# Kernel tuning notes

Hardware: AMD Instinct MI355X
Metric: run time of the kernel (lower is better)

The kernel has to match this reference:

```python
import jax, jax.numpy as jnp
import numpy as np

N, E, D = 100000, 640000, 128

def setup_inputs() -> dict:
    key = jax.random.key(0)
    ks = jax.random.split(key, 12)
    s = 1.0 / np.sqrt(D)
    sg = 1.0 / np.sqrt(2 * D)
    return {
        "nodes": jax.random.normal(ks[0], (N, D), jnp.float32),
        "globals_": jax.random.normal(ks[1], (1, D), jnp.float32),
        "senders": jax.random.randint(ks[2], (E,), 0, N, jnp.int32),
        "receivers": jax.random.randint(ks[3], (E,), 0, N, jnp.int32),
        "W1_w": jax.random.normal(ks[4], (D, D), jnp.float32) * s,
        "W1_b": jnp.zeros((D,), jnp.float32),
        "W2_w": jax.random.normal(ks[5], (D, D), jnp.float32) * s,
        "W2_b": jnp.zeros((D,), jnp.float32),
        "W3_w": jax.random.normal(ks[6], (D, D), jnp.float32) * s,
        "W3_b": jnp.zeros((D,), jnp.float32),
        "Wg_w": jax.random.normal(ks[7], (2 * D, D), jnp.float32) * sg,
        "Wg_b": jnp.zeros((D,), jnp.float32),
    }


def reference(nodes, globals_, senders, receivers,
              W1_w, W1_b, W2_w, W2_b, W3_w, W3_b, Wg_w, Wg_b):
    n = nodes.shape[0]
    # W1 skip-branch projection
    h = nodes @ W1_w + W1_b                              # [N, D]
    # GraphConvolution: W2 projection + symmetric-normalized sum aggregation
    conv = nodes @ W2_w + W2_b                           # [N, D]
    ones = jnp.ones(senders.shape, conv.dtype)
    send_deg = jax.ops.segment_sum(ones, senders, num_segments=n)
    recv_deg = jax.ops.segment_sum(ones, receivers, num_segments=n)
    conv = conv * jax.lax.rsqrt(jnp.maximum(send_deg, 1.0))[:, None]
    agg = jax.ops.segment_sum(conv[senders], receivers, num_segments=n)  # gather + scatter
    agg = agg * jax.lax.rsqrt(jnp.maximum(recv_deg, 1.0))[:, None]
    h = h + agg
    # global -> node broadcast (globals is not None)
    h = h + (globals_[0:1] @ W3_w + W3_b)
    h = jax.nn.relu(h)
    h = h + nodes                                        # residual
    # global update: aggregate nodes (sum over single graph) + gated residual
    an = jnp.sum(h, axis=0, keepdims=True)               # [1, D]
    g_new = globals_ + jax.nn.relu(jnp.concatenate([an, globals_], axis=-1) @ Wg_w + Wg_b)
    return h, g_new
```

## Files before the change

### kernel.cpp

```cpp
#include <hip/hip_runtime.h>

#define D 128
#define AGGB 3136
#define MAXDEG 16
#define OVFCAP 16384

typedef __attribute__((ext_vector_type(8))) short short8;
typedef __attribute__((ext_vector_type(4))) float floatx4;

__device__ inline void bf16split(float x, ushort& hi, ushort& lo) {
  unsigned u = __float_as_uint(x);
  unsigned rh = (u + 0x7FFFu + ((u >> 16) & 1u)) & 0xFFFF0000u;
  hi = (ushort)(rh >> 16);
  float fl = x - __uint_as_float(rh);
  unsigned ul = __float_as_uint(fl);
  lo = (ushort)((ul + 0x7FFFu + ((ul >> 16) & 1u)) >> 16);
}

__device__ inline void place_edge(int s, int r, int p, int* __restrict__ srtp,
                                  int* __restrict__ ovf, int* __restrict__ ovfn) {
  if (p < MAXDEG) {
    srtp[r * MAXDEG + p] = s;
  } else {
    const int q = atomicAdd(ovfn, 1);
    if (q < OVFCAP) {
      ovf[2 * q] = r;
      ovf[2 * q + 1] = s;
    }
  }
}

__global__ void k_prep(const float* __restrict__ g, const float* __restrict__ W3,
                       const float* __restrict__ b3, float* __restrict__ gvec,
                       const float* __restrict__ W1, const float* __restrict__ W2,
                       ushort* __restrict__ wt) {
  const int b = blockIdx.x;
  if (b == 0) {
    __shared__ float part[256];
    const int j = threadIdx.x & 127, half = threadIdx.x >> 7;
    float acc = 0.f;
    for (int k = half * 64; k < half * 64 + 64; ++k)
      acc = fmaf(g[k], W3[k * D + j], acc);
    part[threadIdx.x] = acc;
    __syncthreads();
    if (threadIdx.x < D) gvec[j] = b3[j] + part[j] + part[j + 128];
    return;
  }
  const int id = (b - 1) * 256 + threadIdx.x;
  const int mat = id >> 14, idx = id & 16383;
  const int k = idx >> 7, nn = idx & 127;
  const float x = (mat ? W2 : W1)[k * D + nn];
  ushort hi, lo;
  bf16split(x, hi, lo);
  wt[(size_t)mat * 32768 + (size_t)nn * 128 + k] = hi;
  wt[(size_t)mat * 32768 + 16384 + (size_t)nn * 128 + k] = lo;
}

__global__ __launch_bounds__(256, 6) void k_eg(
    const int* __restrict__ snd, const int* __restrict__ rcv,
    int* __restrict__ cs, int* __restrict__ cr, int* __restrict__ srtp,
    int* __restrict__ ovf, int* __restrict__ ovfn, int E, int nbE4,
    const float* __restrict__ A, const ushort* __restrict__ wt,
    float* __restrict__ h1, int n) {
  const int b = blockIdx.x, t = threadIdx.x;
  if (b < nbE4) {
    const int e0 = b * 1024 + t * 4;
    if (e0 + 3 < E) {
      const int4 s4 = *(const int4*)(snd + e0);
      const int4 r4 = *(const int4*)(rcv + e0);
      atomicAdd(cs + s4.x, 1);
      atomicAdd(cs + s4.y, 1);
      atomicAdd(cs + s4.z, 1);
      atomicAdd(cs + s4.w, 1);
      const int p0 = atomicAdd(cr + r4.x, 1);
      const int p1 = atomicAdd(cr + r4.y, 1);
      const int p2 = atomicAdd(cr + r4.z, 1);
      const int p3 = atomicAdd(cr + r4.w, 1);
      place_edge(s4.x, r4.x, p0, srtp, ovf, ovfn);
      place_edge(s4.y, r4.y, p1, srtp, ovf, ovfn);
      place_edge(s4.z, r4.z, p2, srtp, ovf, ovfn);
      place_edge(s4.w, r4.w, p3, srtp, ovf, ovfn);
    } else {
      for (int e = e0; e < E && e < e0 + 4; ++e) {
        const int s = snd[e], r = rcv[e];
        atomicAdd(cs + s, 1);
        place_edge(s, r, atomicAdd(cr + r, 1), srtp, ovf, ovfn);
      }
    }
    return;
  }
  __shared__ ushort As[2 * 2 * 2560];
  const int row0 = (b - nbE4) * 64;
  const int lane = t & 63, w = t >> 6;
  const int m = lane & 15, quad = lane >> 4;

  floatx4 acc[4][2];
#pragma unroll
  for (int i = 0; i < 4; ++i)
#pragma unroll
    for (int j = 0; j < 2; ++j) acc[i][j] = (floatx4)0.f;

  const int srow = t >> 2, ko = (t & 3) * 8;
  const int grow = min(row0 + srow, n - 1);
  const float* Ag = A + (size_t)grow * D + ko;
  const int sa = srow * 40 + ko;

  float4 f0, f1;
#define LOADP(p)                              \
  {                                           \
    f0 = *(const float4*)(Ag + (p) * 32);     \
    f1 = *(const float4*)(Ag + (p) * 32 + 4); \
  }
#define STOREB(buf)                                               \
  {                                                               \
    ushort h0, l0, h1_, l1_, h2, l2, h3, l3;                      \
    ushort* Bp = &As[(buf) * 5120];                               \
    bf16split(f0.x, h0, l0); bf16split(f0.y, h1_, l1_);           \
    bf16split(f0.z, h2, l2); bf16split(f0.w, h3, l3);             \
    *(ushort4*)&Bp[sa] = make_ushort4(h0, h1_, h2, h3);           \
    *(ushort4*)&Bp[2560 + sa] = make_ushort4(l0, l1_, l2, l3);    \
    bf16split(f1.x, h0, l0); bf16split(f1.y, h1_, l1_);           \
    bf16split(f1.z, h2, l2); bf16split(f1.w, h3, l3);             \
    *(ushort4*)&Bp[sa + 4] = make_ushort4(h0, h1_, h2, h3);       \
    *(ushort4*)&Bp[2560 + sa + 4] = make_ushort4(l0, l1_, l2, l3);\
  }

  LOADP(0);
  STOREB(0);
  LOADP(1);
  __syncthreads();

  for (int p = 0; p < 4; ++p) {
    if (p < 3) STOREB((p + 1) & 1);
    if (p < 2) LOADP(p + 2);
    const ushort* Ab = &As[(p & 1) * 5120];
#pragma unroll
    for (int j = 0; j < 2; ++j) {
      const ushort* g1 = wt + (size_t)(w * 32 + j * 16 + m) * 128 + p * 32 + quad * 8;
      const short8 w1h = *(const short8*)g1;
      const short8 w1l = *(const short8*)(g1 + 16384);
#pragma unroll
      for (int i = 0; i < 4; ++i) {
        const int r = (i * 16 + m) * 40 + quad * 8;
        const short8 a1h = *(const short8*)&Ab[r];
        const short8 a1l = *(const short8*)&Ab[2560 + r];
        floatx4 c = acc[i][j];
        c = __builtin_amdgcn_mfma_f32_16x16x32_bf16(a1h, w1h, c, 0, 0, 0);
        c = __builtin_amdgcn_mfma_f32_16x16x32_bf16(a1h, w1l, c, 0, 0, 0);
        c = __builtin_amdgcn_mfma_f32_16x16x32_bf16(a1l, w1h, c, 0, 0, 0);
        acc[i][j] = c;
      }
    }
    __syncthreads();
  }
#undef LOADP
#undef STOREB

#pragma unroll
  for (int i = 0; i < 4; ++i)
#pragma unroll
    for (int pp = 0; pp < 4; ++pp) {
      const int rg = row0 + i * 16 + quad * 4 + pp;
      if (rg >= n) continue;
#pragma unroll
      for (int j = 0; j < 2; ++j)
        h1[(size_t)rg * D + w * 32 + j * 16 + m] = acc[i][j][pp];
    }
}

__global__ __launch_bounds__(256) void k_agg(
    const float* __restrict__ nodes, int* __restrict__ cnt_recv,
    const int* __restrict__ cnt_send, const int* __restrict__ srtp,
    const int* __restrict__ ovf, const int* __restrict__ ovfn,
    ushort* __restrict__ yh, ushort* __restrict__ yl, int n) {
  float* cf = (float*)cnt_recv;
  const int hw = threadIdx.x >> 5, ln = threadIdx.x & 31;
  const int ghw = blockIdx.x * 8 + hw;
  const int nhw = AGGB * 8;
  const int c0 = ln * 4;

  for (int r0 = ghw; r0 < n; r0 += 2 * nhw) {
    const int r1 = r0 + nhw;
    const bool has1 = r1 < n;
    const int dg0 = cnt_recv[r0];
    const int dg1 = has1 ? cnt_recv[r1] : 0;
    const int base0 = r0 * MAXDEG;
    const int base1 = (has1 ? r1 : 0) * MAXDEG;

    const int4 qa0 = *(const int4*)(srtp + base0);
    const int4 qb0 = *(const int4*)(srtp + base0 + 4);
    const int4 qa1 = *(const int4*)(srtp + base1);
    const int4 qb1 = *(const int4*)(srtp + base1 + 4);
    int idx0[8] = {qa0.x, qa0.y, qa0.z, qa0.w, qb0.x, qb0.y, qb0.z, qb0.w};
    int idx1[8] = {qa1.x, qa1.y, qa1.z, qa1.w, qb1.x, qb1.y, qb1.z, qb1.w};
#pragma unroll
    for (int j = 0; j < 8; ++j) {
      idx0[j] = (j < dg0) ? idx0[j] : 0;
      idx1[j] = (j < dg1) ? idx1[j] : 0;
    }
    float4 g0[8], g1[8];
#pragma unroll
    for (int j = 0; j < 8; ++j)
      g0[j] = *(const float4*)(nodes + (size_t)idx0[j] * D + c0);
#pragma unroll
    for (int j = 0; j < 8; ++j)
      g1[j] = *(const float4*)(nodes + (size_t)idx1[j] * D + c0);
    float rs0[8], rs1[8];
#pragma unroll
    for (int j = 0; j < 8; ++j) {
      rs0[j] = (j < dg0) ? rsqrtf(fmaxf((float)cnt_send[idx0[j]], 1.f)) : 0.f;
      rs1[j] = (j < dg1) ? rsqrtf(fmaxf((float)cnt_send[idx1[j]], 1.f)) : 0.f;
    }

    float sx0 = 0.f, sy0 = 0.f, sz0 = 0.f, sw0 = 0.f, cs0 = 0.f;
    float sx1 = 0.f, sy1 = 0.f, sz1 = 0.f, sw1 = 0.f, cs1 = 0.f;
#pragma unroll
    for (int j = 0; j < 8; ++j) {
      sx0 = fmaf(rs0[j], g0[j].x, sx0);
      sy0 = fmaf(rs0[j], g0[j].y, sy0);
      sz0 = fmaf(rs0[j], g0[j].z, sz0);
      sw0 = fmaf(rs0[j], g0[j].w, sw0);
      cs0 += rs0[j];
      sx1 = fmaf(rs1[j], g1[j].x, sx1);
      sy1 = fmaf(rs1[j], g1[j].y, sy1);
      sz1 = fmaf(rs1[j], g1[j].z, sz1);
      sw1 = fmaf(rs1[j], g1[j].w, sw1);
      cs1 += rs1[j];
    }
    for (int i = 8; i < min(dg0, MAXDEG); ++i) {
      const int s = srtp[base0 + i];
      const float r = rsqrtf(fmaxf((float)cnt_send[s], 1.f));
      const float4 c = *(const float4*)(nodes + (size_t)s * D + c0);
      sx0 = fmaf(r, c.x, sx0); sy0 = fmaf(r, c.y, sy0);
      sz0 = fmaf(r, c.z, sz0); sw0 = fmaf(r, c.w, sw0);
      cs0 += r;
    }
    for (int i = 8; i < min(dg1, MAXDEG); ++i) {
      const int s = srtp[base1 + i];
      const float r = rsqrtf(fmaxf((float)cnt_send[s], 1.f));
      const float4 c = *(const float4*)(nodes + (size_t)s * D + c0);
      sx1 = fmaf(r, c.x, sx1); sy1 = fmaf(r, c.y, sy1);
      sz1 = fmaf(r, c.z, sz1); sw1 = fmaf(r, c.w, sw1);
      cs1 += r;
    }
    if (dg0 > MAXDEG) {
      const int novf = min(*ovfn, OVFCAP);
      for (int k2 = 0; k2 < novf; ++k2) {
        if (ovf[2 * k2] == r0) {
          const int s = ovf[2 * k2 + 1];
          const float r = rsqrtf(fmaxf((float)cnt_send[s], 1.f));
          const float4 c = *(const float4*)(nodes + (size_t)s * D + c0);
          sx0 = fmaf(r, c.x, sx0); sy0 = fmaf(r, c.y, sy0);
          sz0 = fmaf(r, c.z, sz0); sw0 = fmaf(r, c.w, sw0);
          cs0 += r;
        }
      }
    }
    if (dg1 > MAXDEG) {
      const int novf = min(*ovfn, OVFCAP);
      for (int k2 = 0; k2 < novf; ++k2) {
        if (ovf[2 * k2] == r1) {
          const int s = ovf[2 * k2 + 1];
          const float r = rsqrtf(fmaxf((float)cnt_send[s], 1.f));
          const float4 c = *(const float4*)(nodes + (size_t)s * D + c0);
          sx1 = fmaf(r, c.x, sx1); sy1 = fmaf(r, c.y, sy1);
          sz1 = fmaf(r, c.z, sz1); sw1 = fmaf(r, c.w, sw1);
          cs1 += r;
        }
      }
    }

    {
      const float rr = rsqrtf(fmaxf((float)dg0, 1.f));
      ushort h0, l0, h1, l1, h2, l2, h3, l3;
      bf16split(sx0 * rr, h0, l0);
      bf16split(sy0 * rr, h1, l1);
      bf16split(sz0 * rr, h2, l2);
      bf16split(sw0 * rr, h3, l3);
      *(ushort4*)(yh + (size_t)r0 * D + c0) = make_ushort4(h0, h1, h2, h3);
      *(ushort4*)(yl + (size_t)r0 * D + c0) = make_ushort4(l0, l1, l2, l3);
      if (ln == 0) cf[r0] = rr * cs0;
    }
    if (has1) {
      const float rr = rsqrtf(fmaxf((float)dg1, 1.f));
      ushort h0, l0, h1, l1, h2, l2, h3, l3;
      bf16split(sx1 * rr, h0, l0);
      bf16split(sy1 * rr, h1, l1);
      bf16split(sz1 * rr, h2, l2);
      bf16split(sw1 * rr, h3, l3);
      *(ushort4*)(yh + (size_t)r1 * D + c0) = make_ushort4(h0, h1, h2, h3);
      *(ushort4*)(yl + (size_t)r1 * D + c0) = make_ushort4(l0, l1, l2, l3);
      if (ln == 0) cf[r1] = rr * cs1;
    }
  }
}

__global__ __launch_bounds__(256, 6) void k_gemm2(
    const float* __restrict__ A, const ushort* __restrict__ yh,
    const ushort* __restrict__ yl, const ushort* __restrict__ wt,
    const float* __restrict__ b1, const float* __restrict__ b2,
    const float* __restrict__ gvec, const float* __restrict__ cf,
    float* hio, float* __restrict__ an, int n) {
  __shared__ ushort As[2 * 2 * 2560];
  const int t = threadIdx.x;
  const int row0 = blockIdx.x * 64;
  const int lane = t & 63, w = t >> 6;
  const int m = lane & 15, quad = lane >> 4;

  floatx4 acc[4][2];
#pragma unroll
  for (int i = 0; i < 4; ++i)
#pragma unroll
    for (int j = 0; j < 2; ++j) acc[i][j] = (floatx4)0.f;

  const int srow = t >> 2, ko = (t & 3) * 8;
  const int grow = min(row0 + srow, n - 1);
  const ushort* yhb = yh + (size_t)grow * D + ko;
  const ushort* ylb = yl + (size_t)grow * D + ko;
  const int sa = srow * 40 + ko;

  uint4 r2, r3;
#define LOADP(p)                          \
  {                                       \
    r2 = *(const uint4*)(yhb + (p) * 32); \
    r3 = *(const uint4*)(ylb + (p) * 32); \
  }
#define STOREB(buf)                 \
  {                                 \
    ushort* Bp = &As[(buf) * 5120]; \
    *(uint4*)&Bp[sa] = r2;          \
    *(uint4*)&Bp[2560 + sa] = r3;   \
  }

  LOADP(0);
  STOREB(0);
  LOADP(1);
  __syncthreads();

  for (int p = 0; p < 4; ++p) {
    if (p < 3) STOREB((p + 1) & 1);
    if (p < 2) LOADP(p + 2);
    const ushort* Ab = &As[(p & 1) * 5120];
#pragma unroll
    for (int j = 0; j < 2; ++j) {
      const ushort* g2 =
          wt + 32768 + (size_t)(w * 32 + j * 16 + m) * 128 + p * 32 + quad * 8;
      const short8 w2h = *(const short8*)g2;
      const short8 w2l = *(const short8*)(g2 + 16384);
#pragma unroll
      for (int i = 0; i < 4; ++i) {
        const int r = (i * 16 + m) * 40 + quad * 8;
        const short8 a2h = *(const short8*)&Ab[r];
        const short8 a2l = *(const short8*)&Ab[2560 + r];
        floatx4 c = acc[i][j];
        c = __builtin_amdgcn_mfma_f32_16x16x32_bf16(a2h, w2h, c, 0, 0, 0);
        c = __builtin_amdgcn_mfma_f32_16x16x32_bf16(a2h, w2l, c, 0, 0, 0);
        c = __builtin_amdgcn_mfma_f32_16x16x32_bf16(a2l, w2h, c, 0, 0, 0);
        acc[i][j] = c;
      }
    }
    __syncthreads();
  }
#undef LOADP
#undef STOREB

  float bb[2], b2c[2];
#pragma unroll
  for (int j = 0; j < 2; ++j) {
    const int col = w * 32 + j * 16 + m;
    bb[j] = b1[col] + gvec[col];
    b2c[j] = b2[col];
  }
  float asum[2] = {0.f, 0.f};
#pragma unroll
  for (int i = 0; i < 4; ++i)
#pragma unroll
    for (int pp = 0; pp < 4; ++pp) {
      const int rg = row0 + i * 16 + quad * 4 + pp;
      if (rg >= n) continue;
      const float crv = cf[rg];
#pragma unroll
      for (int j = 0; j < 2; ++j) {
        const int col = w * 32 + j * 16 + m;
        float v = acc[i][j][pp] + bb[j] + crv * b2c[j] + hio[(size_t)rg * D + col];
        v = fmaxf(v, 0.f) + A[(size_t)rg * D + col];
        hio[(size_t)rg * D + col] = v;
        asum[j] += v;
      }
    }
#pragma unroll
  for (int j = 0; j < 2; ++j) {
    float v = asum[j];
    v += __shfl_xor(v, 16);
    v += __shfl_xor(v, 32);
    if (lane < 16) atomicAdd(an + w * 32 + j * 16 + m, v);
  }
}

__global__ void k_gupdate(const float* __restrict__ an, const float* __restrict__ g,
                          const float* __restrict__ Wg, const float* __restrict__ bg,
                          float* __restrict__ gout) {
  __shared__ float part[256];
  const int j = threadIdx.x & 127, half = threadIdx.x >> 7;
  float acc = 0.f;
  if (half == 0) {
    for (int k = 0; k < D; ++k) acc = fmaf(an[k], Wg[k * D + j], acc);
  } else {
    for (int k = 0; k < D; ++k) acc = fmaf(g[k], Wg[(D + k) * D + j], acc);
  }
  part[threadIdx.x] = acc;
  __syncthreads();
  if (threadIdx.x < D)
    gout[j] = g[j] + fmaxf(bg[j] + part[j] + part[j + 128], 0.f);
}

extern "C" void kernel_launch(void* const* d_in, const int* in_sizes, int n_in,
                              void* d_out, int out_size, void* d_ws, size_t ws_size,
                              hipStream_t stream) {
  const float* nodes = (const float*)d_in[0];
  const float* globals_ = (const float*)d_in[1];
  const int* senders = (const int*)d_in[2];
  const int* receivers = (const int*)d_in[3];
  const float* W1_w = (const float*)d_in[4];
  const float* W1_b = (const float*)d_in[5];
  const float* W2_w = (const float*)d_in[6];
  const float* W2_b = (const float*)d_in[7];
  const float* W3_w = (const float*)d_in[8];
  const float* W3_b = (const float*)d_in[9];
  const float* Wg_w = (const float*)d_in[10];
  const float* Wg_b = (const float*)d_in[11];
  const int N = in_sizes[0] / D;
  const int E = in_sizes[2];
  const int nbE4 = (E + 1023) / 1024;
  const int NG = (N + 63) / 64;

  float* h = (float*)d_out;
  float* gout = h + (size_t)N * D;

  float* ws = (float*)d_ws;
  ushort* yh = (ushort*)ws;
  ushort* yl = yh + (size_t)N * D;
  int* cnt_send = (int*)(yl + (size_t)N * D);
  int* cnt_recv = cnt_send + N;
  float* an = (float*)(cnt_recv + N);
  int* ovfn = (int*)(an + D);
  float* gvec = (float*)(ovfn + 64);
  int* srtp = (int*)(gvec + D);
  int* ovf = srtp + (size_t)N * MAXDEG;
  ushort* wt = (ushort*)(ovf + 2 * OVFCAP);

  (void)hipMemsetAsync(cnt_send, 0, (size_t)(2 * N + D + 64) * sizeof(int), stream);

  hipLaunchKernelGGL(k_prep, dim3(129), dim3(256), 0, stream,
                     globals_, W3_w, W3_b, gvec, W1_w, W2_w, wt);
  hipLaunchKernelGGL(k_eg, dim3(nbE4 + NG), dim3(256), 0, stream,
                     senders, receivers, cnt_send, cnt_recv, srtp, ovf, ovfn,
                     E, nbE4, nodes, wt, h, N);
  hipLaunchKernelGGL(k_agg, dim3(AGGB), dim3(256), 0, stream,
                     nodes, cnt_recv, cnt_send, srtp, ovf, ovfn, yh, yl, N);
  hipLaunchKernelGGL(k_gemm2, dim3(NG), dim3(256), 0, stream,
                     nodes, yh, yl, wt, W1_b, W2_b, gvec,
                     (const float*)cnt_recv, h, an, N);
  hipLaunchKernelGGL(k_gupdate, dim3(1), dim3(256), 0, stream, an, globals_,
                     Wg_w, Wg_b, gout);
}
```

Measured before the change: 376.5 us.

## Fuse all stages into one persistent kernel with grid barriers and merged GEMM

Replaces the five-kernel pipeline with a single persistent kernel of 512 blocks that uses atomic grid-wide barriers between the prep, edge-bucketing, aggregation and GEMM phases. It also merges the two GEMMs (nodes@W1 and agg@W2) into one pass, so the intermediate h is no longer written and re-read. The goal is to remove launch gaps and one full N×D round trip. In exchange, the edge-bucketing work no longer overlaps with the first GEMM. The spin barriers assume all 512 blocks are co-resident (2 per CU), which risks deadlock if that does not hold, and the fixed grid may underuse the GPU in some phases.

```diff
diff --git a/kernel.cpp b/kernel.cpp
--- a/kernel.cpp
+++ b/kernel.cpp
@@ -1,9 +1,9 @@
 #include <hip/hip_runtime.h>
 
 #define D 128
-#define AGGB 3136
 #define MAXDEG 16
 #define OVFCAP 16384
+#define GRID 512
 
 typedef __attribute__((ext_vector_type(8))) short short8;
 typedef __attribute__((ext_vector_type(4))) float floatx4;
@@ -17,8 +17,8 @@
   lo = (ushort)((ul + 0x7FFFu + ((ul >> 16) & 1u)) >> 16);
 }
 
-__device__ inline void place_edge(int s, int r, int p, int* __restrict__ srtp,
-                                  int* __restrict__ ovf, int* __restrict__ ovfn) {
+__device__ inline void place_edge(int s, int r, int p, int* srtp, int* ovf,
+                                  int* ovfn) {
   if (p < MAXDEG) {
     srtp[r * MAXDEG + p] = s;
   } else {
@@ -30,41 +30,59 @@
   }
 }
 
-__global__ void k_prep(const float* __restrict__ g, const float* __restrict__ W3,
-                       const float* __restrict__ b3, float* __restrict__ gvec,
-                       const float* __restrict__ W1, const float* __restrict__ W2,
-                       ushort* __restrict__ wt) {
-  const int b = blockIdx.x;
-  if (b == 0) {
-    __shared__ float part[256];
-    const int j = threadIdx.x & 127, half = threadIdx.x >> 7;
+__device__ inline void gbar(int* bar, int target) {
+  __syncthreads();
+  if (threadIdx.x == 0) {
+    __hip_atomic_fetch_add(bar, 1, __ATOMIC_RELEASE, __HIP_MEMORY_SCOPE_AGENT);
+    while (__hip_atomic_load(bar, __ATOMIC_ACQUIRE, __HIP_MEMORY_SCOPE_AGENT) <
+           target)
+      __builtin_amdgcn_s_sleep(2);
+  }
+  __syncthreads();
+}
+
+__global__ __launch_bounds__(256, 2) void k_mega(
+    const float* __restrict__ nodes, const float* __restrict__ g,
+    const int* __restrict__ snd, const int* __restrict__ rcv,
+    const float* __restrict__ W1, const float* __restrict__ b1,
+    const float* __restrict__ W2, const float* __restrict__ b2,
+    const float* __restrict__ W3, const float* __restrict__ b3,
+    const float* __restrict__ Wg, const float* __restrict__ bg,
+    int* cs, int* cr, float* an, int* ctrl, float* gvec, int* srtp, int* ovf,
+    ushort* wt, ushort* yh, ushort* yl, float* h, float* gout, int E, int n) {
+  __shared__ ushort As[2 * 4 * 2560];
+  int* ovfn = ctrl;
+  int* bar = ctrl + 1;
+  const int b = blockIdx.x, t = threadIdx.x;
+  const int gtid = b * 256 + t;
+  const int lane = t & 63, w = t >> 6;
+  const int m = lane & 15, quad = lane >> 4;
+  const int nbE4 = (E + 1023) / 1024;
+  const int nT = (n + 63) / 64;
+
+  if (gtid < 32768) {
+    const int mat = gtid >> 14, idx = gtid & 16383;
+    const int k = idx >> 7, nn = idx & 127;
+    const float x = (mat ? W2 : W1)[k * D + nn];
+    ushort hi, lo;
+    bf16split(x, hi, lo);
+    wt[(size_t)mat * 32768 + (size_t)nn * 128 + k] = hi;
+    wt[(size_t)mat * 32768 + 16384 + (size_t)nn * 128 + k] = lo;
+  }
+  if (b == GRID - 1) {
+    float* part = (float*)As;
+    const int j = t & 127, half = t >> 7;
     float acc = 0.f;
     for (int k = half * 64; k < half * 64 + 64; ++k)
       acc = fmaf(g[k], W3[k * D + j], acc);
-    part[threadIdx.x] = acc;
+    part[t] = acc;
     __syncthreads();
-    if (threadIdx.x < D) gvec[j] = b3[j] + part[j] + part[j + 128];
-    return;
-  }
-  const int id = (b - 1) * 256 + threadIdx.x;
-  const int mat = id >> 14, idx = id & 16383;
-  const int k = idx >> 7, nn = idx & 127;
-  const float x = (mat ? W2 : W1)[k * D + nn];
-  ushort hi, lo;
-  bf16split(x, hi, lo);
-  wt[(size_t)mat * 32768 + (size_t)nn * 128 + k] = hi;
-  wt[(size_t)mat * 32768 + 16384 + (size_t)nn * 128 + k] = lo;
-}
-
-__global__ __launch_bounds__(256, 6) void k_eg(
-    const int* __restrict__ snd, const int* __restrict__ rcv,
-    int* __restrict__ cs, int* __restrict__ cr, int* __restrict__ srtp,
-    int* __restrict__ ovf, int* __restrict__ ovfn, int E, int nbE4,
-    const float* __restrict__ A, const ushort* __restrict__ wt,
-    float* __restrict__ h1, int n) {
-  const int b = blockIdx.x, t = threadIdx.x;
-  if (b < nbE4) {
-    const int e0 = b * 1024 + t * 4;
+    if (t < D) gvec[j] = b3[j] + part[j] + part[j + 128];
+  }
+  gbar(bar, GRID);
+
+  for (int c = b; c < nbE4; c += GRID) {
+    const int e0 = c * 1024 + t * 4;
     if (e0 + 3 < E) {
       const int4 s4 = *(const int4*)(snd + e0);
       const int4 r4 = *(const int4*)(rcv + e0);
@@ -87,34 +105,167 @@
         place_edge(s, r, atomicAdd(cr + r, 1), srtp, ovf, ovfn);
       }
     }
-    return;
-  }
-  __shared__ ushort As[2 * 2 * 2560];
-  const int row0 = (b - nbE4) * 64;
-  const int lane = t & 63, w = t >> 6;
-  const int m = lane & 15, quad = lane >> 4;
-
-  floatx4 acc[4][2];
-#pragma unroll
-  for (int i = 0; i < 4; ++i)
-#pragma unroll
-    for (int j = 0; j < 2; ++j) acc[i][j] = (floatx4)0.f;
-
-  const int srow = t >> 2, ko = (t & 3) * 8;
-  const int grow = min(row0 + srow, n - 1);
-  const float* Ag = A + (size_t)grow * D + ko;
-  const int sa = srow * 40 + ko;
-
-  float4 f0, f1;
+  }
+  gbar(bar, 2 * GRID);
+
+  {
+    float* cf = (float*)cr;
+    const int hw = t >> 5, ln = t & 31;
+    const int ghw = b * 8 + hw;
+    const int nhw = GRID * 8;
+    const int c0 = ln * 4;
+    for (int r0 = ghw; r0 < n; r0 += 2 * nhw) {
+      const int r1 = r0 + nhw;
+      const bool has1 = r1 < n;
+      const int dg0 = cr[r0];
+      const int dg1 = has1 ? cr[r1] : 0;
+      const int base0 = r0 * MAXDEG;
+      const int base1 = (has1 ? r1 : 0) * MAXDEG;
+
+      const int4 qa0 = *(const int4*)(srtp + base0);
+      const int4 qb0 = *(const int4*)(srtp + base0 + 4);
+      const int4 qa1 = *(const int4*)(srtp + base1);
+      const int4 qb1 = *(const int4*)(srtp + base1 + 4);
+      int idx0[8] = {qa0.x, qa0.y, qa0.z, qa0.w, qb0.x, qb0.y, qb0.z, qb0.w};
+      int idx1[8] = {qa1.x, qa1.y, qa1.z, qa1.w, qb1.x, qb1.y, qb1.z, qb1.w};
+#pragma unroll
+      for (int j = 0; j < 8; ++j) {
+        idx0[j] = (j < dg0) ? idx0[j] : 0;
+        idx1[j] = (j < dg1) ? idx1[j] : 0;
+      }
+      float4 g0[8], g1[8];
+#pragma unroll
+      for (int j = 0; j < 8; ++j)
+        g0[j] = *(const float4*)(nodes + (size_t)idx0[j] * D + c0);
+#pragma unroll
+      for (int j = 0; j < 8; ++j)
+        g1[j] = *(const float4*)(nodes + (size_t)idx1[j] * D + c0);
+      float rs0[8], rs1[8];
+#pragma unroll
+      for (int j = 0; j < 8; ++j) {
+        rs0[j] = (j < dg0) ? rsqrtf(fmaxf((float)cs[idx0[j]], 1.f)) : 0.f;
+        rs1[j] = (j < dg1) ? rsqrtf(fmaxf((float)cs[idx1[j]], 1.f)) : 0.f;
+      }
+      float sx0 = 0.f, sy0 = 0.f, sz0 = 0.f, sw0 = 0.f, cs0 = 0.f;
+      float sx1 = 0.f, sy1 = 0.f, sz1 = 0.f, sw1 = 0.f, cs1 = 0.f;
+#pragma unroll
+      for (int j = 0; j < 8; ++j) {
+        sx0 = fmaf(rs0[j], g0[j].x, sx0);
+        sy0 = fmaf(rs0[j], g0[j].y, sy0);
+        sz0 = fmaf(rs0[j], g0[j].z, sz0);
+        sw0 = fmaf(rs0[j], g0[j].w, sw0);
+        cs0 += rs0[j];
+        sx1 = fmaf(rs1[j], g1[j].x, sx1);
+        sy1 = fmaf(rs1[j], g1[j].y, sy1);
+        sz1 = fmaf(rs1[j], g1[j].z, sz1);
+        sw1 = fmaf(rs1[j], g1[j].w, sw1);
+        cs1 += rs1[j];
+      }
+      for (int i = 8; i < min(dg0, MAXDEG); ++i) {
+        const int s = srtp[base0 + i];
+        const float r = rsqrtf(fmaxf((float)cs[s], 1.f));
+        const float4 c = *(const float4*)(nodes + (size_t)s * D + c0);
+        sx0 = fmaf(r, c.x, sx0); sy0 = fmaf(r, c.y, sy0);
+        sz0 = fmaf(r, c.z, sz0); sw0 = fmaf(r, c.w, sw0);
+        cs0 += r;
+      }
+      for (int i = 8; i < min(dg1, MAXDEG); ++i) {
+        const int s = srtp[base1 + i];
+        const float r = rsqrtf(fmaxf((float)cs[s], 1.f));
+        const float4 c = *(const float4*)(nodes + (size_t)s * D + c0);
+        sx1 = fmaf(r, c.x, sx1); sy1 = fmaf(r, c.y, sy1);
+        sz1 = fmaf(r, c.z, sz1); sw1 = fmaf(r, c.w, sw1);
+        cs1 += r;
+      }
+      if (dg0 > MAXDEG) {
+        const int novf = min(ctrl[0], OVFCAP);
+        for (int k2 = 0; k2 < novf; ++k2)
+          if (ovf[2 * k2] == r0) {
+            const int s = ovf[2 * k2 + 1];
+            const float r = rsqrtf(fmaxf((float)cs[s], 1.f));
+            const float4 c = *(const float4*)(nodes + (size_t)s * D + c0);
+            sx0 = fmaf(r, c.x, sx0); sy0 = fmaf(r, c.y, sy0);
+            sz0 = fmaf(r, c.z, sz0); sw0 = fmaf(r, c.w, sw0);
+            cs0 += r;
+          }
+      }
+      if (dg1 > MAXDEG) {
+        const int novf = min(ctrl[0], OVFCAP);
+        for (int k2 = 0; k2 < novf; ++k2)
+          if (ovf[2 * k2] == r1) {
+            const int s = ovf[2 * k2 + 1];
+            const float r = rsqrtf(fmaxf((float)cs[s], 1.f));
+            const float4 c = *(const float4*)(nodes + (size_t)s * D + c0);
+            sx1 = fmaf(r, c.x, sx1); sy1 = fmaf(r, c.y, sy1);
+            sz1 = fmaf(r, c.z, sz1); sw1 = fmaf(r, c.w, sw1);
+            cs1 += r;
+          }
+      }
+      {
+        const float rr = rsqrtf(fmaxf((float)dg0, 1.f));
+        ushort h0, l0, h1, l1, h2, l2, h3, l3;
+        bf16split(sx0 * rr, h0, l0);
+        bf16split(sy0 * rr, h1, l1);
+        bf16split(sz0 * rr, h2, l2);
+        bf16split(sw0 * rr, h3, l3);
+        *(ushort4*)(yh + (size_t)r0 * D + c0) = make_ushort4(h0, h1, h2, h3);
+        *(ushort4*)(yl + (size_t)r0 * D + c0) = make_ushort4(l0, l1, l2, l3);
+        if (ln == 0) cf[r0] = rr * cs0;
+      }
+      if (has1) {
+        const float rr = rsqrtf(fmaxf((float)dg1, 1.f));
+        ushort h0, l0, h1, l1, h2, l2, h3, l3;
+        bf16split(sx1 * rr, h0, l0);
+        bf16split(sy1 * rr, h1, l1);
+        bf16split(sz1 * rr, h2, l2);
+        bf16split(sw1 * rr, h3, l3);
+        *(ushort4*)(yh + (size_t)r1 * D + c0) = make_ushort4(h0, h1, h2, h3);
+        *(ushort4*)(yl + (size_t)r1 * D + c0) = make_ushort4(l0, l1, l2, l3);
+        if (ln == 0) cf[r1] = rr * cs1;
+      }
+    }
+  }
+  gbar(bar, 3 * GRID);
+
+  {
+    const float* cf = (const float*)cr;
+    float bb[2], b2c[2];
+#pragma unroll
+    for (int j = 0; j < 2; ++j) {
+      const int col = w * 32 + j * 16 + m;
+      bb[j] = b1[col] + gvec[col];
+      b2c[j] = b2[col];
+    }
+    float asum[2] = {0.f, 0.f};
+
+    for (int tile = b; tile < nT; tile += GRID) {
+      const int row0 = tile * 64;
+      floatx4 acc[4][2];
+#pragma unroll
+      for (int i = 0; i < 4; ++i)
+#pragma unroll
+        for (int j = 0; j < 2; ++j) acc[i][j] = (floatx4)0.f;
+
+      const int srow = t >> 2, ko = (t & 3) * 8;
+      const int grow = min(row0 + srow, n - 1);
+      const float* Ag = nodes + (size_t)grow * D + ko;
+      const ushort* yhb = yh + (size_t)grow * D + ko;
+      const ushort* ylb = yl + (size_t)grow * D + ko;
+      const int sa = srow * 40 + ko;
+
+      float4 f0, f1;
+      uint4 r2, r3;
 #define LOADP(p)                              \
   {                                           \
     f0 = *(const float4*)(Ag + (p) * 32);     \
     f1 = *(const float4*)(Ag + (p) * 32 + 4); \
+    r2 = *(const uint4*)(yhb + (p) * 32);     \
+    r3 = *(const uint4*)(ylb + (p) * 32);     \
   }
 #define STOREB(buf)                                               \
   {                                                               \
     ushort h0, l0, h1_, l1_, h2, l2, h3, l3;                      \
-    ushort* Bp = &As[(buf) * 5120];                               \
+    ushort* Bp = &As[(buf) * 10240];                              \
     bf16split(f0.x, h0, l0); bf16split(f0.y, h1_, l1_);           \
     bf16split(f0.z, h2, l2); bf16split(f0.w, h3, l3);             \
     *(ushort4*)&Bp[sa] = make_ushort4(h0, h1_, h2, h3);           \
@@ -123,295 +274,99 @@
     bf16split(f1.z, h2, l2); bf16split(f1.w, h3, l3);             \
     *(ushort4*)&Bp[sa + 4] = make_ushort4(h0, h1_, h2, h3);       \
     *(ushort4*)&Bp[2560 + sa + 4] = make_ushort4(l0, l1_, l2, l3);\
-  }
-
-  LOADP(0);
-  STOREB(0);
-  LOADP(1);
-  __syncthreads();
-
-  for (int p = 0; p < 4; ++p) {
-    if (p < 3) STOREB((p + 1) & 1);
-    if (p < 2) LOADP(p + 2);
-    const ushort* Ab = &As[(p & 1) * 5120];
-#pragma unroll
-    for (int j = 0; j < 2; ++j) {
-      const ushort* g1 = wt + (size_t)(w * 32 + j * 16 + m) * 128 + p * 32 + quad * 8;
-      const short8 w1h = *(const short8*)g1;
-      const short8 w1l = *(const short8*)(g1 + 16384);
-#pragma unroll
-      for (int i = 0; i < 4; ++i) {
-        const int r = (i * 16 + m) * 40 + quad * 8;
-        const short8 a1h = *(const short8*)&Ab[r];
-        const short8 a1l = *(const short8*)&Ab[2560 + r];
-        floatx4 c = acc[i][j];
-        c = __builtin_amdgcn_mfma_f32_16x16x32_bf16(a1h, w1h, c, 0, 0, 0);
-        c = __builtin_amdgcn_mfma_f32_16x16x32_bf16(a1h, w1l, c, 0, 0, 0);
-        c = __builtin_amdgcn_mfma_f32_16x16x32_bf16(a1l, w1h, c, 0, 0, 0);
-        acc[i][j] = c;
-      }
-    }
-    __syncthreads();
-  }
+    *(uint4*)&Bp[5120 + sa] = r2;                                 \
+    *(uint4*)&Bp[7680 + sa] = r3;                                 \
+  }
+
+      LOADP(0);
+      STOREB(0);
+      LOADP(1);
+      __syncthreads();
+
+      for (int p = 0; p < 4; ++p) {
+        if (p < 3) STOREB((p + 1) & 1);
+        if (p < 2) LOADP(p + 2);
+        const ushort* Ab = &As[(p & 1) * 10240];
+#pragma unroll
+        for (int j = 0; j < 2; ++j) {
+          const ushort* g1 =
+              wt + (size_t)(w * 32 + j * 16 + m) * 128 + p * 32 + quad * 8;
+          const short8 w1h = *(const short8*)g1;
+          const short8 w1l = *(const short8*)(g1 + 16384);
+          const short8 w2h = *(const short8*)(g1 + 32768);
+          const short8 w2l = *(const short8*)(g1 + 49152);
+#pragma unroll
+          for (int i = 0; i < 4; ++i) {
+            const int r = (i * 16 + m) * 40 + quad * 8;
+            const short8 a1h = *(const short8*)&Ab[r];
+            const short8 a1l = *(const short8*)&Ab[2560 + r];
+            const short8 a2h = *(const short8*)&Ab[5120 + r];
+            const short8 a2l = *(const short8*)&Ab[7680 + r];
+            floatx4 c = acc[i][j];
+            c = __builtin_amdgcn_mfma_f32_16x16x32_bf16(a1h, w1h, c, 0, 0, 0);
+            c = __builtin_amdgcn_mfma_f32_16x16x32_bf16(a1h, w1l, c, 0, 0, 0);
+            c = __builtin_amdgcn_mfma_f32_16x16x32_bf16(a1l, w1h, c, 0, 0, 0);
+            c = __builtin_amdgcn_mfma_f32_16x16x32_bf16(a2h, w2h, c, 0, 0, 0);
+            c = __builtin_amdgcn_mfma_f32_16x16x32_bf16(a2h, w2l, c, 0, 0, 0);
+            c = __builtin_amdgcn_mfma_f32_16x16x32_bf16(a2l, w2h, c, 0, 0, 0);
+            acc[i][j] = c;
+          }
+        }
+        __syncthreads();
+      }
 #undef LOADP
 #undef STOREB
 
 #pragma unroll
-  for (int i = 0; i < 4; ++i)
-#pragma unroll
-    for (int pp = 0; pp < 4; ++pp) {
-      const int rg = row0 + i * 16 + quad * 4 + pp;
-      if (rg >= n) continue;
-#pragma unroll
-      for (int j = 0; j < 2; ++j)
-        h1[(size_t)rg * D + w * 32 + j * 16 + m] = acc[i][j][pp];
-    }
-}
-
-__global__ __launch_bounds__(256) void k_agg(
-    const float* __restrict__ nodes, int* __restrict__ cnt_recv,
-    const int* __restrict__ cnt_send, const int* __restrict__ srtp,
-    const int* __restrict__ ovf, const int* __restrict__ ovfn,
-    ushort* __restrict__ yh, ushort* __restrict__ yl, int n) {
-  float* cf = (float*)cnt_recv;
-  const int hw = threadIdx.x >> 5, ln = threadIdx.x & 31;
-  const int ghw = blockIdx.x * 8 + hw;
-  const int nhw = AGGB * 8;
-  const int c0 = ln * 4;
-
-  for (int r0 = ghw; r0 < n; r0 += 2 * nhw) {
-    const int r1 = r0 + nhw;
-    const bool has1 = r1 < n;
-    const int dg0 = cnt_recv[r0];
-    const int dg1 = has1 ? cnt_recv[r1] : 0;
-    const int base0 = r0 * MAXDEG;
-    const int base1 = (has1 ? r1 : 0) * MAXDEG;
-
-    const int4 qa0 = *(const int4*)(srtp + base0);
-    const int4 qb0 = *(const int4*)(srtp + base0 + 4);
-    const int4 qa1 = *(const int4*)(srtp + base1);
-    const int4 qb1 = *(const int4*)(srtp + base1 + 4);
-    int idx0[8] = {qa0.x, qa0.y, qa0.z, qa0.w, qb0.x, qb0.y, qb0.z, qb0.w};
-    int idx1[8] = {qa1.x, qa1.y, qa1.z, qa1.w, qb1.x, qb1.y, qb1.z, qb1.w};
-#pragma unroll
-    for (int j = 0; j < 8; ++j) {
-      idx0[j] = (j < dg0) ? idx0[j] : 0;
-      idx1[j] = (j < dg1) ? idx1[j] : 0;
-    }
-    float4 g0[8], g1[8];
-#pragma unroll
-    for (int j = 0; j < 8; ++j)
-      g0[j] = *(const float4*)(nodes + (size_t)idx0[j] * D + c0);
-#pragma unroll
-    for (int j = 0; j < 8; ++j)
-      g1[j] = *(const float4*)(nodes + (size_t)idx1[j] * D + c0);
-    float rs0[8], rs1[8];
-#pragma unroll
-    for (int j = 0; j < 8; ++j) {
-      rs0[j] = (j < dg0) ? rsqrtf(fmaxf((float)cnt_send[idx0[j]], 1.f)) : 0.f;
-      rs1[j] = (j < dg1) ? rsqrtf(fmaxf((float)cnt_send[idx1[j]], 1.f)) : 0.f;
-    }
-
-    float sx0 = 0.f, sy0 = 0.f, sz0 = 0.f, sw0 = 0.f, cs0 = 0.f;
-    float sx1 = 0.f, sy1 = 0.f, sz1 = 0.f, sw1 = 0.f, cs1 = 0.f;
-#pragma unroll
-    for (int j = 0; j < 8; ++j) {
-      sx0 = fmaf(rs0[j], g0[j].x, sx0);
-      sy0 = fmaf(rs0[j], g0[j].y, sy0);
-      sz0 = fmaf(rs0[j], g0[j].z, sz0);
-      sw0 = fmaf(rs0[j], g0[j].w, sw0);
-      cs0 += rs0[j];
-      sx1 = fmaf(rs1[j], g1[j].x, sx1);
-      sy1 = fmaf(rs1[j], g1[j].y, sy1);
-      sz1 = fmaf(rs1[j], g1[j].z, sz1);
-      sw1 = fmaf(rs1[j], g1[j].w, sw1);
-      cs1 += rs1[j];
-    }
-    for (int i = 8; i < min(dg0, MAXDEG); ++i) {
-      const int s = srtp[base0 + i];
-      const float r = rsqrtf(fmaxf((float)cnt_send[s], 1.f));
-      const float4 c = *(const float4*)(nodes + (size_t)s * D + c0);
-      sx0 = fmaf(r, c.x, sx0); sy0 = fmaf(r, c.y, sy0);
-      sz0 = fmaf(r, c.z, sz0); sw0 = fmaf(r, c.w, sw0);
-      cs0 += r;
-    }
-    for (int i = 8; i < min(dg1, MAXDEG); ++i) {
-      const int s = srtp[base1 + i];
-      const float r = rsqrtf(fmaxf((float)cnt_send[s], 1.f));
-      const float4 c = *(const float4*)(nodes + (size_t)s * D + c0);
-      sx1 = fmaf(r, c.x, sx1); sy1 = fmaf(r, c.y, sy1);
-      sz1 = fmaf(r, c.z, sz1); sw1 = fmaf(r, c.w, sw1);
-      cs1 += r;
-    }
-    if (dg0 > MAXDEG) {
-      const int novf = min(*ovfn, OVFCAP);
-      for (int k2 = 0; k2 < novf; ++k2) {
-        if (ovf[2 * k2] == r0) {
-          const int s = ovf[2 * k2 + 1];
-          const float r = rsqrtf(fmaxf((float)cnt_send[s], 1.f));
-          const float4 c = *(const float4*)(nodes + (size_t)s * D + c0);
-          sx0 = fmaf(r, c.x, sx0); sy0 = fmaf(r, c.y, sy0);
-          sz0 = fmaf(r, c.z, sz0); sw0 = fmaf(r, c.w, sw0);
-          cs0 += r;
+      for (int i = 0; i < 4; ++i)
+#pragma unroll
+        for (int pp = 0; pp < 4; ++pp) {
+          const int rg = row0 + i * 16 + quad * 4 + pp;
+          if (rg >= n) continue;
+          const float crv = cf[rg];
+#pragma unroll
+          for (int j = 0; j < 2; ++j) {
+            const int col = w * 32 + j * 16 + m;
+            float v = acc[i][j][pp] + bb[j] + crv * b2c[j];
+            v = fmaxf(v, 0.f) + nodes[(size_t)rg * D + col];
+            h[(size_t)rg * D + col] = v;
+            asum[j] += v;
+          }
         }
-      }
-    }
-    if (dg1 > MAXDEG) {
-      const int novf = min(*ovfn, OVFCAP);
-      for (int k2 = 0; k2 < novf; ++k2) {
-        if (ovf[2 * k2] == r1) {
-          const int s = ovf[2 * k2 + 1];
-          const float r = rsqrtf(fmaxf((float)cnt_send[s], 1.f));
-          const float4 c = *(const float4*)(nodes + (size_t)s * D + c0);
-          sx1 = fmaf(r, c.x, sx1); sy1 = fmaf(r, c.y, sy1);
-          sz1 = fmaf(r, c.z, sz1); sw1 = fmaf(r, c.w, sw1);
-          cs1 += r;
-        }
-      }
-    }
-
-    {
-      const float rr = rsqrtf(fmaxf((float)dg0, 1.f));
-      ushort h0, l0, h1, l1, h2, l2, h3, l3;
-      bf16split(sx0 * rr, h0, l0);
-      bf16split(sy0 * rr, h1, l1);
-      bf16split(sz0 * rr, h2, l2);
-      bf16split(sw0 * rr, h3, l3);
-      *(ushort4*)(yh + (size_t)r0 * D + c0) = make_ushort4(h0, h1, h2, h3);
-      *(ushort4*)(yl + (size_t)r0 * D + c0) = make_ushort4(l0, l1, l2, l3);
-      if (ln == 0) cf[r0] = rr * cs0;
-    }
-    if (has1) {
-      const float rr = rsqrtf(fmaxf((float)dg1, 1.f));
-      ushort h0, l0, h1, l1, h2, l2, h3, l3;
-      bf16split(sx1 * rr, h0, l0);
-      bf16split(sy1 * rr, h1, l1);
-      bf16split(sz1 * rr, h2, l2);
-      bf16split(sw1 * rr, h3, l3);
-      *(ushort4*)(yh + (size_t)r1 * D + c0) = make_ushort4(h0, h1, h2, h3);
-      *(ushort4*)(yl + (size_t)r1 * D + c0) = make_ushort4(l0, l1, l2, l3);
-      if (ln == 0) cf[r1] = rr * cs1;
-    }
-  }
-}
-
-__global__ __launch_bounds__(256, 6) void k_gemm2(
-    const float* __restrict__ A, const ushort* __restrict__ yh,
-    const ushort* __restrict__ yl, const ushort* __restrict__ wt,
-    const float* __restrict__ b1, const float* __restrict__ b2,
-    const float* __restrict__ gvec, const float* __restrict__ cf,
-    float* hio, float* __restrict__ an, int n) {
-  __shared__ ushort As[2 * 2 * 2560];
-  const int t = threadIdx.x;
-  const int row0 = blockIdx.x * 64;
-  const int lane = t & 63, w = t >> 6;
-  const int m = lane & 15, quad = lane >> 4;
-
-  floatx4 acc[4][2];
-#pragma unroll
-  for (int i = 0; i < 4; ++i)
-#pragma unroll
-    for (int j = 0; j < 2; ++j) acc[i][j] = (floatx4)0.f;
-
-  const int srow = t >> 2, ko = (t & 3) * 8;
-  const int grow = min(row0 + srow, n - 1);
-  const ushort* yhb = yh + (size_t)grow * D + ko;
-  const ushort* ylb = yl + (size_t)grow * D + ko;
-  const int sa = srow * 40 + ko;
-
-  uint4 r2, r3;
-#define LOADP(p)                          \
-  {                                       \
-    r2 = *(const uint4*)(yhb + (p) * 32); \
-    r3 = *(const uint4*)(ylb + (p) * 32); \
-  }
-#define STOREB(buf)                 \
-  {                                 \
-    ushort* Bp = &As[(buf) * 5120]; \
-    *(uint4*)&Bp[sa] = r2;          \
-    *(uint4*)&Bp[2560 + sa] = r3;   \
-  }
-
-  LOADP(0);
-  STOREB(0);
-  LOADP(1);
+    }
+#pragma unroll
+    for (int j = 0; j < 2; ++j) {
+      float v = asum[j];
+      v += __shfl_xor(v, 16);
+      v += __shfl_xor(v, 32);
+      if (lane < 16) atomicAdd(an + w * 32 + j * 16 + m, v);
+    }
+  }
+
   __syncthreads();
-
-  for (int p = 0; p < 4; ++p) {
-    if (p < 3) STOREB((p + 1) & 1);
-    if (p < 2) LOADP(p + 2);
-    const ushort* Ab = &As[(p & 1) * 5120];
-#pragma unroll
-    for (int j = 0; j < 2; ++j) {
-      const ushort* g2 =
-          wt + 32768 + (size_t)(w * 32 + j * 16 + m) * 128 + p * 32 + quad * 8;
-      const short8 w2h = *(const short8*)g2;
-      const short8 w2l = *(const short8*)(g2 + 16384);
-#pragma unroll
-      for (int i = 0; i < 4; ++i) {
-        const int r = (i * 16 + m) * 40 + quad * 8;
-        const short8 a2h = *(const short8*)&Ab[r];
-        const short8 a2l = *(const short8*)&Ab[2560 + r];
-        floatx4 c = acc[i][j];
-        c = __builtin_amdgcn_mfma_f32_16x16x32_bf16(a2h, w2h, c, 0, 0, 0);
-        c = __builtin_amdgcn_mfma_f32_16x16x32_bf16(a2h, w2l, c, 0, 0, 0);
-        c = __builtin_amdgcn_mfma_f32_16x16x32_bf16(a2l, w2h, c, 0, 0, 0);
-        acc[i][j] = c;
-      }
-    }
+  if (t == 0)
+    __hip_atomic_fetch_add(bar, 1, __ATOMIC_RELEASE, __HIP_MEMORY_SCOPE_AGENT);
+  if (b != 0) return;
+  if (t == 0) {
+    while (__hip_atomic_load(bar, __ATOMIC_ACQUIRE, __HIP_MEMORY_SCOPE_AGENT) <
+           4 * GRID)
+      __builtin_amdgcn_s_sleep(2);
+  }
+  __syncthreads();
+  {
+    float* part = (float*)As;
+    const int j = t & 127, half = t >> 7;
+    float acc = 0.f;
+    if (half == 0) {
+      for (int k = 0; k < D; ++k) acc = fmaf(an[k], Wg[k * D + j], acc);
+    } else {
+      for (int k = 0; k < D; ++k) acc = fmaf(g[k], Wg[(D + k) * D + j], acc);
+    }
+    part[t] = acc;
     __syncthreads();
-  }
-#undef LOADP
-#undef STOREB
-
-  float bb[2], b2c[2];
-#pragma unroll
-  for (int j = 0; j < 2; ++j) {
-    const int col = w * 32 + j * 16 + m;
-    bb[j] = b1[col] + gvec[col];
-    b2c[j] = b2[col];
-  }
-  float asum[2] = {0.f, 0.f};
-#pragma unroll
-  for (int i = 0; i < 4; ++i)
-#pragma unroll
-    for (int pp = 0; pp < 4; ++pp) {
-      const int rg = row0 + i * 16 + quad * 4 + pp;
-      if (rg >= n) continue;
-      const float crv = cf[rg];
-#pragma unroll
-      for (int j = 0; j < 2; ++j) {
-        const int col = w * 32 + j * 16 + m;
-        float v = acc[i][j][pp] + bb[j] + crv * b2c[j] + hio[(size_t)rg * D + col];
-        v = fmaxf(v, 0.f) + A[(size_t)rg * D + col];
-        hio[(size_t)rg * D + col] = v;
-        asum[j] += v;
-      }
-    }
-#pragma unroll
-  for (int j = 0; j < 2; ++j) {
-    float v = asum[j];
-    v += __shfl_xor(v, 16);
-    v += __shfl_xor(v, 32);
-    if (lane < 16) atomicAdd(an + w * 32 + j * 16 + m, v);
-  }
-}
-
-__global__ void k_gupdate(const float* __restrict__ an, const float* __restrict__ g,
-                          const float* __restrict__ Wg, const float* __restrict__ bg,
-                          float* __restrict__ gout) {
-  __shared__ float part[256];
-  const int j = threadIdx.x & 127, half = threadIdx.x >> 7;
-  float acc = 0.f;
-  if (half == 0) {
-    for (int k = 0; k < D; ++k) acc = fmaf(an[k], Wg[k * D + j], acc);
-  } else {
-    for (int k = 0; k < D; ++k) acc = fmaf(g[k], Wg[(D + k) * D + j], acc);
-  }
-  part[threadIdx.x] = acc;
-  __syncthreads();
-  if (threadIdx.x < D)
-    gout[j] = g[j] + fmaxf(bg[j] + part[j] + part[j + 128], 0.f);
+    if (t < D)
+      gout[j] = g[j] + fmaxf(bg[j] + part[j] + part[j + 128], 0.f);
+  }
 }
 
 extern "C" void kernel_launch(void* const* d_in, const int* in_sizes, int n_in,
@@ -431,8 +386,6 @@
   const float* Wg_b = (const float*)d_in[11];
   const int N = in_sizes[0] / D;
   const int E = in_sizes[2];
-  const int nbE4 = (E + 1023) / 1024;
-  const int NG = (N + 63) / 64;
 
   float* h = (float*)d_out;
   float* gout = h + (size_t)N * D;
@@ -440,27 +393,20 @@
   float* ws = (float*)d_ws;
   ushort* yh = (ushort*)ws;
   ushort* yl = yh + (size_t)N * D;
-  int* cnt_send = (int*)(yl + (size_t)N * D);
-  int* cnt_recv = cnt_send + N;
-  float* an = (float*)(cnt_recv + N);
-  int* ovfn = (int*)(an + D);
-  float* gvec = (float*)(ovfn + 64);
+  int* cs = (int*)(yl + (size_t)N * D);
+  int* cr = cs + N;
+  float* an = (float*)(cr + N);
+  int* ctrl = (int*)(an + D);
+  float* gvec = (float*)(ctrl + 64);
   int* srtp = (int*)(gvec + D);
   int* ovf = srtp + (size_t)N * MAXDEG;
   ushort* wt = (ushort*)(ovf + 2 * OVFCAP);
 
-  (void)hipMemsetAsync(cnt_send, 0, (size_t)(2 * N + D + 64) * sizeof(int), stream);
-
-  hipLaunchKernelGGL(k_prep, dim3(129), dim3(256), 0, stream,
-                     globals_, W3_w, W3_b, gvec, W1_w, W2_w, wt);
-  hipLaunchKernelGGL(k_eg, dim3(nbE4 + NG), dim3(256), 0, stream,
-                     senders, receivers, cnt_send, cnt_recv, srtp, ovf, ovfn,
-                     E, nbE4, nodes, wt, h, N);
-  hipLaunchKernelGGL(k_agg, dim3(AGGB), dim3(256), 0, stream,
-                     nodes, cnt_recv, cnt_send, srtp, ovf, ovfn, yh, yl, N);
-  hipLaunchKernelGGL(k_gemm2, dim3(NG), dim3(256), 0, stream,
-                     nodes, yh, yl, wt, W1_b, W2_b, gvec,
-                     (const float*)cnt_recv, h, an, N);
-  hipLaunchKernelGGL(k_gupdate, dim3(1), dim3(256), 0, stream, an, globals_,
-                     Wg_w, Wg_b, gout);
+  (void)hipMemsetAsync(cs, 0, (size_t)(2 * N + D + 64) * sizeof(int), stream);
+
+  hipLaunchKernelGGL(k_mega, dim3(GRID), dim3(256), 0, stream,
+                     nodes, globals_, senders, receivers,
+                     W1_w, W1_b, W2_w, W2_b, W3_w, W3_b, Wg_w, Wg_b,
+                     cs, cr, an, ctrl, gvec, srtp, ovf, wt, yh, yl,
+                     h, gout, E, N);
 }
```

Measured after the change: 725.0 us. 1.93x slower.
